# Kernel optimization log

Hardware: AMD Instinct MI355X
Metric: run time of the kernel (lower is better)

Reference implementation:

```python
import jax, jax.numpy as jnp
import numpy as np

B, S, H = 2, 1024, 2048
E, F = 16, 1024          # num_experts, moe_intermediate_size
TOP_K = 4
SH_F = 5632              # shared_expert_intermediate_size


def setup_inputs() -> dict:
    key = jax.random.key(0)
    ks = jax.random.split(key, 9)
    sc = 0.02
    return {
        'hidden_states': jax.random.normal(ks[0], (B, S, H), dtype=jnp.float32),
        'w_router': jax.random.normal(ks[1], (H, E), dtype=jnp.float32) * sc,
        'w_gate': jax.random.normal(ks[2], (E, H, F), dtype=jnp.float32) * sc,
        'w_up': jax.random.normal(ks[3], (E, H, F), dtype=jnp.float32) * sc,
        'w_down': jax.random.normal(ks[4], (E, F, H), dtype=jnp.float32) * sc,
        'w_sh_gate': jax.random.normal(ks[5], (H, SH_F), dtype=jnp.float32) * sc,
        'w_sh_up': jax.random.normal(ks[6], (H, SH_F), dtype=jnp.float32) * sc,
        'w_sh_down': jax.random.normal(ks[7], (SH_F, H), dtype=jnp.float32) * sc,
        'w_sh_expert_gate': jax.random.normal(ks[8], (H, 1), dtype=jnp.float32) * sc,
    }


def reference(hidden_states, w_router, w_gate, w_up, w_down,
              w_sh_gate, w_sh_up, w_sh_down, w_sh_expert_gate):
    b, s, h = hidden_states.shape
    x = hidden_states.reshape(-1, h)                      # [T, H]

    # router: softmax over all experts, then top-k, renormalize (norm_topk_prob=True)
    router_logits = x @ w_router                          # [T, E]
    probs = jax.nn.softmax(router_logits, axis=-1)
    topk_w, topk_ids = jax.lax.top_k(probs, TOP_K)        # [T, k]
    topk_w = topk_w / jnp.sum(topk_w, axis=-1, keepdims=True)

    # combine matrix [T, E]: routing weight per (token, expert)
    combine = jnp.sum(
        jax.nn.one_hot(topk_ids, E, dtype=x.dtype) * topk_w[..., None], axis=1)

    # experts: SwiGLU per expert, weighted-combined before down projection
    g = jnp.einsum('th,ehf->tef', x, w_gate)              # [T, E, F]
    u = jnp.einsum('th,ehf->tef', x, w_up)
    act = jax.nn.silu(g) * u                              # SiluAndMul
    act = act * combine[:, :, None]                       # fold routing weights
    moe_out = jnp.einsum('tef,efh->th', act, w_down)      # [T, H]

    # shared expert with sigmoid gate
    sg = jax.nn.silu(x @ w_sh_gate) * (x @ w_sh_up)       # [T, SH_F]
    shared = sg @ w_sh_down                               # [T, H]
    gate = jax.nn.sigmoid(x @ w_sh_expert_gate)           # [T, 1]
    out = moe_out + gate * shared
    return out.reshape(b, s, h)
```

## Files before the change

kernel.cpp:

```cpp
#include <hip/hip_runtime.h>
#include <hip/hip_bf16.h>
#include <stdint.h>

#define T_TOK 2048
#define HD    2048
#define NE    16
#define FF    1024
#define TOPK  4
#define SHF   5632

typedef __attribute__((ext_vector_type(8))) short short8;
typedef __attribute__((ext_vector_type(4))) float f32x4;

typedef const __attribute__((address_space(1))) uint32_t* gp1_t;
typedef __attribute__((address_space(3))) uint32_t* lp3_t;

__device__ __forceinline__ void gload_lds16(const void* g, void* l) {
  __builtin_amdgcn_global_load_lds((gp1_t)g, (lp3_t)l, 16, 0, 0);
}

__device__ __forceinline__ unsigned short f2bf(float f) {
  __hip_bfloat16 h = __float2bfloat16(f);
  return __builtin_bit_cast(unsigned short, h);
}
__device__ __forceinline__ float bf2f(unsigned short u) {
  return __uint_as_float(((uint32_t)u) << 16);
}

__global__ __launch_bounds__(256) void k_prep(const float* __restrict__ x,
                                              unsigned short* __restrict__ xb,
                                              float* __restrict__ out,
                                              int* __restrict__ counts, int n) {
  int i = blockIdx.x * blockDim.x + threadIdx.x;
  int stride = gridDim.x * blockDim.x;
  for (; i < n; i += stride) { xb[i] = f2bf(x[i]); out[i] = 0.f; }
  if (blockIdx.x == 0 && threadIdx.x < NE) counts[threadIdx.x] = 0;
}

__global__ __launch_bounds__(256) void k_transpose(const float* __restrict__ src,
    unsigned short* __restrict__ dst, int K, int N) {
  __shared__ unsigned short tile[64][72];
  const int k0 = blockIdx.x * 64;
  const int n0 = blockIdx.y * 64;
  const size_t boff = (size_t)blockIdx.z * K * N;
  src += boff; dst += boff;
  const int t = threadIdx.x;
  const int c4 = (t & 15) * 4;
  const int kr0 = (t >> 4) * 4;
#pragma unroll
  for (int j = 0; j < 4; ++j) {
    int kr = kr0 + j;
    float4 v = *(const float4*)(src + (size_t)(k0 + kr) * N + n0 + c4);
    tile[c4 + 0][kr] = f2bf(v.x);
    tile[c4 + 1][kr] = f2bf(v.y);
    tile[c4 + 2][kr] = f2bf(v.z);
    tile[c4 + 3][kr] = f2bf(v.w);
  }
  __syncthreads();
  const int nr = t >> 2;
  const int kc = (t & 3) * 8;
  unsigned short* orow = dst + (size_t)(n0 + nr) * K + k0;
  *(short8*)(orow + kc)      = *(const short8*)(&tile[nr][kc]);
  *(short8*)(orow + kc + 32) = *(const short8*)(&tile[nr][kc + 32]);
}

__global__ __launch_bounds__(64) void k_router(
    const float* __restrict__ x, const float* __restrict__ wr,
    const float* __restrict__ wsg, int* __restrict__ counts,
    int* __restrict__ list, float* __restrict__ wlist,
    float* __restrict__ gate_sh) {
  const int t = blockIdx.x;
  const int lane = threadIdx.x;
  const float* xrow = x + (size_t)t * HD;
  float p[NE + 1];
#pragma unroll
  for (int e = 0; e <= NE; ++e) p[e] = 0.f;
  for (int i = lane; i < HD; i += 64) {
    float xv = xrow[i];
    const float* wrow = wr + (size_t)i * NE;
#pragma unroll
    for (int e = 0; e < NE; ++e) p[e] += xv * wrow[e];
    p[NE] += xv * wsg[i];
  }
#pragma unroll
  for (int e = 0; e <= NE; ++e) {
    float v = p[e];
    for (int off = 32; off; off >>= 1) v += __shfl_xor(v, off);
    p[e] = v;
  }
  if (lane == 0) {
    gate_sh[t] = 1.f / (1.f + __expf(-p[NE]));
    float l[NE];
#pragma unroll
    for (int e = 0; e < NE; ++e) l[e] = p[e];
    int ids[TOPK]; float lg[TOPK];
#pragma unroll
    for (int k = 0; k < TOPK; ++k) {
      int best = 0; float bv = l[0];
#pragma unroll
      for (int e = 1; e < NE; ++e) { if (l[e] > bv) { bv = l[e]; best = e; } }
      ids[k] = best; lg[k] = bv; l[best] = -1e30f;
    }
    float m = lg[0], s = 0.f, w[TOPK];
#pragma unroll
    for (int k = 0; k < TOPK; ++k) { w[k] = __expf(lg[k] - m); s += w[k]; }
    float inv = 1.f / s;
#pragma unroll
    for (int k = 0; k < TOPK; ++k) {
      int e = ids[k];
      int pos = atomicAdd(&counts[e], 1);
      list[e * T_TOK + pos] = t;
      wlist[e * T_TOK + pos] = w[k] * inv;
    }
  }
}

__global__ __launch_bounds__(256) void k_offsets(
    const int* __restrict__ counts, int* __restrict__ offsets,
    const float* __restrict__ wlist, float* __restrict__ wpair) {
  __shared__ int soff[NE];
  if (threadIdx.x == 0) {
    int off = 0;
    for (int e = 0; e < NE; ++e) { offsets[e] = off; soff[e] = off; off += counts[e]; }
    offsets[NE] = off;
  }
  __syncthreads();
  for (int idx = threadIdx.x; idx < NE * T_TOK; idx += 256) {
    int e = idx >> 11, pos = idx & (T_TOK - 1);
    if (pos < counts[e]) wpair[soff[e] + pos] = wlist[idx];
  }
}

template<int MODE>
__global__ __launch_bounds__(256, 2) void k_gemm(
    const unsigned short* __restrict__ A, int lda, int nkt,
    const unsigned short* __restrict__ B0, const unsigned short* __restrict__ B1,
    int nsplit, size_t strideB, int ldb,
    unsigned short* __restrict__ O0, unsigned short* __restrict__ O1, int ldo,
    float* __restrict__ OF,
    const int* __restrict__ offsets, const int* __restrict__ counts,
    const int* __restrict__ list, const float* __restrict__ gate_sh)
{
  __shared__ unsigned short lds[2][2 * 8192];
  __shared__ int tokLDS[128];

  const int cb = blockIdx.x, rb = blockIdx.y;
  const int e = (MODE <= 1) ? blockIdx.z : 0;
  const int tid = threadIdx.x, l = tid & 63, wid = tid >> 6;
  const int wr = wid >> 1, wc = wid & 1;

  int cnt = T_TOK;
  if (MODE <= 1) {
    cnt = counts[e];
    if (rb * 128 >= cnt) return;
  }
  if (MODE == 0) {
    if (tid < 128) {
      int r = rb * 128 + tid;
      tokLDS[tid] = list[e * T_TOK + (r < cnt ? r : cnt - 1)];
    }
    __syncthreads();
  }

  const int swz8 = ((l & 7) ^ (l >> 3)) * 8;
  const unsigned short* Bsel = (cb < nsplit) ? B0 : B1;
  const int cb2 = (cb < nsplit) ? cb : cb - nsplit;
  const size_t eoff = (MODE <= 1) ? (size_t)e * strideB : (size_t)0;

  const unsigned short* aS[4];
  const unsigned short* bS[4];
#pragma unroll
  for (int i = 0; i < 4; ++i) {
    int rloc = wid * 32 + i * 8 + (l >> 3);
    int arow;
    if (MODE == 0) arow = tokLDS[rloc];
    else if (MODE == 1) { int rr = rb * 128 + rloc; if (rr >= cnt) rr = cnt - 1; arow = offsets[e] + rr; }
    else arow = rb * 128 + rloc;
    aS[i] = A + (size_t)arow * lda + swz8;
    bS[i] = Bsel + eoff + (size_t)(cb2 * 128 + rloc) * ldb + swz8;
  }

  auto STAGE = [&](int kt) {
    unsigned short* base = &lds[kt & 1][0] + (wid * 32) * 64;
    const int k0 = kt * 64;
#pragma unroll
    for (int i = 0; i < 4; ++i) {
      gload_lds16(aS[i] + k0, base + i * 8 * 64);
      gload_lds16(bS[i] + k0, base + i * 8 * 64 + 8192);
    }
  };

  f32x4 acc[4][4];
#pragma unroll
  for (int mf = 0; mf < 4; ++mf)
#pragma unroll
    for (int nf = 0; nf < 4; ++nf) acc[mf][nf] = (f32x4){0.f, 0.f, 0.f, 0.f};

  STAGE(0);

  for (int kt = 0; kt < nkt; ++kt) {
    if (kt + 1 < nkt) {
      STAGE(kt + 1);
      asm volatile("s_waitcnt vmcnt(8)" ::: "memory");
    } else {
      asm volatile("s_waitcnt vmcnt(0)" ::: "memory");
    }
    __builtin_amdgcn_s_barrier();
    asm volatile("" ::: "memory");

    const char* lAb = (const char*)&lds[kt & 1][0];
    const char* lBb = lAb + 16384;
#pragma unroll
    for (int kk = 0; kk < 2; ++kk) {
      const int kb = kk * 64 + ((l >> 4) * 16);
      short8 af[4], bf[4];
#pragma unroll
      for (int mf = 0; mf < 4; ++mf) {
        int row = wr * 64 + mf * 16 + (l & 15);
        af[mf] = *(const short8*)(lAb + row * 128 + (kb ^ ((row & 7) << 4)));
      }
#pragma unroll
      for (int nf = 0; nf < 4; ++nf) {
        int n = wc * 64 + nf * 16 + (l & 15);
        bf[nf] = *(const short8*)(lBb + n * 128 + (kb ^ ((n & 7) << 4)));
      }
      __builtin_amdgcn_s_setprio(1);
#pragma unroll
      for (int mf = 0; mf < 4; ++mf)
#pragma unroll
        for (int nf = 0; nf < 4; ++nf)
          acc[mf][nf] = __builtin_amdgcn_mfma_f32_16x16x32_bf16(af[mf], bf[nf], acc[mf][nf], 0, 0, 0);
      __builtin_amdgcn_s_setprio(0);
    }
    asm volatile("" ::: "memory");
    __builtin_amdgcn_s_barrier();
    asm volatile("" ::: "memory");
  }

  const int g4 = (l >> 4) * 4;
  const int cL = l & 15;
  const int colb = cb2 * 128 + wc * 64 + cL;

  if constexpr (MODE == 0) {
    unsigned short* Out = (cb < nsplit) ? O0 : O1;
    const int obase = offsets[e];
#pragma unroll
    for (int mf = 0; mf < 4; ++mf)
#pragma unroll
      for (int r = 0; r < 4; ++r) {
        int rloc = rb * 128 + wr * 64 + mf * 16 + g4 + r;
        if (rloc < cnt) {
          size_t orow = (size_t)(obase + rloc) * ldo + colb;
#pragma unroll
          for (int nf = 0; nf < 4; ++nf)
            Out[orow + nf * 16] = f2bf(acc[mf][nf][r]);
        }
      }
  } else if constexpr (MODE == 2) {
    unsigned short* Out = (cb < nsplit) ? O0 : O1;
#pragma unroll
    for (int mf = 0; mf < 4; ++mf)
#pragma unroll
      for (int r = 0; r < 4; ++r) {
        int rloc = rb * 128 + wr * 64 + mf * 16 + g4 + r;
        size_t orow = (size_t)rloc * ldo + colb;
#pragma unroll
        for (int nf = 0; nf < 4; ++nf)
          Out[orow + nf * 16] = f2bf(acc[mf][nf][r]);
      }
  } else if constexpr (MODE == 1) {
#pragma unroll
    for (int mf = 0; mf < 4; ++mf)
#pragma unroll
      for (int r = 0; r < 4; ++r) {
        int rloc = rb * 128 + wr * 64 + mf * 16 + g4 + r;
        if (rloc < cnt) {
          int tok = list[e * T_TOK + rloc];
          float* dst = OF + (size_t)tok * HD + colb;
#pragma unroll
          for (int nf = 0; nf < 4; ++nf)
            atomicAdd(dst + nf * 16, acc[mf][nf][r]);
        }
      }
  } else {
#pragma unroll
    for (int mf = 0; mf < 4; ++mf)
#pragma unroll
      for (int r = 0; r < 4; ++r) {
        int rloc = rb * 128 + wr * 64 + mf * 16 + g4 + r;
        float g = gate_sh[rloc];
        float* dst = OF + (size_t)rloc * HD + colb;
#pragma unroll
        for (int nf = 0; nf < 4; ++nf)
          dst[nf * 16] += g * acc[mf][nf][r];
      }
  }
}

__global__ __launch_bounds__(256) void k_silu(
    unsigned short* __restrict__ gq, const unsigned short* __restrict__ uq,
    const float* __restrict__ wrow, long total)
{
  long i = ((long)blockIdx.x * blockDim.x + threadIdx.x) * 4;
  const long stride = (long)gridDim.x * blockDim.x * 4;
  for (; i < total; i += stride) {
    ushort4 gv = *(const ushort4*)(gq + i);
    ushort4 uv = *(const ushort4*)(uq + i);
    float w = wrow ? wrow[i >> 10] : 1.f;
    float a0 = bf2f(gv.x), a1 = bf2f(gv.y), a2 = bf2f(gv.z), a3 = bf2f(gv.w);
    float b0 = bf2f(uv.x), b1 = bf2f(uv.y), b2 = bf2f(uv.z), b3 = bf2f(uv.w);
    ushort4 o;
    o.x = f2bf(a0 / (1.f + __expf(-a0)) * b0 * w);
    o.y = f2bf(a1 / (1.f + __expf(-a1)) * b1 * w);
    o.z = f2bf(a2 / (1.f + __expf(-a2)) * b2 * w);
    o.w = f2bf(a3 / (1.f + __expf(-a3)) * b3 * w);
    *(ushort4*)(gq + i) = o;
  }
}

extern "C" void kernel_launch(void* const* d_in, const int* in_sizes, int n_in,
                              void* d_out, int out_size, void* d_ws, size_t ws_size,
                              hipStream_t stream) {
  const float* x     = (const float*)d_in[0];
  const float* wrout = (const float*)d_in[1];
  const float* wgate = (const float*)d_in[2];
  const float* wup   = (const float*)d_in[3];
  const float* wdown = (const float*)d_in[4];
  const float* wsg   = (const float*)d_in[5];
  const float* wsu   = (const float*)d_in[6];
  const float* wsd   = (const float*)d_in[7];
  const float* wseg  = (const float*)d_in[8];
  float* out = (float*)d_out;

  char* ws = (char*)d_ws;
  unsigned short* xb = (unsigned short*)ws;
  char* region1 = ws + (size_t)(8u << 20);
  unsigned short* actg = (unsigned short*)region1;
  unsigned short* actu = (unsigned short*)(region1 + (size_t)(16u << 20));
  unsigned short* sgg  = (unsigned short*)region1;
  unsigned short* sgu  = (unsigned short*)(region1 + (size_t)23068672);
  char* p3 = region1 + (size_t)46137344;
  int*   counts  = (int*)p3;
  int*   offsets = (int*)(p3 + 256);
  float* gateS   = (float*)(p3 + 512);
  float* wpair   = (float*)(p3 + 512 + 8192);
  int*   list    = (int*)(p3 + 512 + 8192 + 32768);
  float* wlist   = (float*)(p3 + 512 + 8192 + 32768 + 131072);
  char* p4 = p3 + (size_t)(1u << 20);
  unsigned short* W1 = (unsigned short*)p4;
  unsigned short* W2 = (unsigned short*)(p4 + (size_t)(64u << 20));
  (void)ws_size; (void)in_sizes; (void)n_in; (void)out_size;

  const int n = T_TOK * HD;
  k_prep<<<dim3(4096), dim3(256), 0, stream>>>(x, xb, out, counts, n);
  k_router<<<dim3(T_TOK), dim3(64), 0, stream>>>(x, wrout, wseg, counts, list, wlist, gateS);
  k_offsets<<<dim3(1), dim3(256), 0, stream>>>(counts, offsets, wlist, wpair);

  k_transpose<<<dim3(32, 16, 16), dim3(256), 0, stream>>>(wgate, W1, HD, FF);
  k_transpose<<<dim3(32, 16, 16), dim3(256), 0, stream>>>(wup,   W2, HD, FF);

  k_gemm<0><<<dim3(16, 16, 16), dim3(256), 0, stream>>>(
      xb, HD, 32, W1, W2, 8, (size_t)HD * FF, HD,
      actg, actu, FF, (float*)nullptr, offsets, counts, list, (const float*)nullptr);
  k_silu<<<dim3(4096), dim3(256), 0, stream>>>(actg, actu, wpair, (long)T_TOK * TOPK * FF);

  k_transpose<<<dim3(16, 32, 16), dim3(256), 0, stream>>>(wdown, W1, FF, HD);
  k_gemm<1><<<dim3(16, 16, 16), dim3(256), 0, stream>>>(
      actg, FF, 16, W1, W1, 1 << 30, (size_t)FF * HD, FF,
      (unsigned short*)nullptr, (unsigned short*)nullptr, HD,
      out, offsets, counts, list, (const float*)nullptr);

  unsigned short* WsgT = W2;
  unsigned short* WsuT = W2 + (size_t)SHF * HD;
  k_transpose<<<dim3(32, 88, 1), dim3(256), 0, stream>>>(wsg, WsgT, HD, SHF);
  k_transpose<<<dim3(32, 88, 1), dim3(256), 0, stream>>>(wsu, WsuT, HD, SHF);

  k_gemm<2><<<dim3(88, 16, 1), dim3(256), 0, stream>>>(
      xb, HD, 32, WsgT, WsuT, 44, (size_t)0, HD,
      sgg, sgu, SHF, (float*)nullptr, offsets, counts, list, (const float*)nullptr);
  k_silu<<<dim3(4096), dim3(256), 0, stream>>>(sgg, sgu, (const float*)nullptr, (long)T_TOK * SHF);

  k_transpose<<<dim3(88, 32, 1), dim3(256), 0, stream>>>(wsd, W1, SHF, HD);
  k_gemm<3><<<dim3(16, 16, 1), dim3(256), 0, stream>>>(
      sgg, SHF, 88, W1, W1, 1 << 30, (size_t)0, SHF,
      (unsigned short*)nullptr, (unsigned short*)nullptr, HD,
      out, offsets, counts, list, gateS);
}
```

Before: 709.8 us.

## Fuse SiLU into up-projection GEMM epilogue and reorder shared/routed expert stages

The two standalone SiLU-multiply kernels are removed. Gate and up projections now run as separate GEMM launches, and the up GEMM's epilogue reads the stored gate result, applies silu(g)*u, and scales by the routing weight. The shared expert now runs first and writes `out` directly instead of accumulating, so the zero-fill in prep goes away and the routed experts then atomically add on top. The gate/up GEMMs drop double buffering and the occupancy hint, using a single LDS buffer with __syncthreads. This trades the elementwise passes and the out-zeroing for an extra GEMM launch, a re-read of the gate tensor, and possibly less load/compute overlap in those GEMMs.

```diff
diff --git a/kernel.cpp b/kernel.cpp
--- a/kernel.cpp
+++ b/kernel.cpp
@@ -29,11 +29,10 @@
 
 __global__ __launch_bounds__(256) void k_prep(const float* __restrict__ x,
                                               unsigned short* __restrict__ xb,
-                                              float* __restrict__ out,
                                               int* __restrict__ counts, int n) {
   int i = blockIdx.x * blockDim.x + threadIdx.x;
   int stride = gridDim.x * blockDim.x;
-  for (; i < n; i += stride) { xb[i] = f2bf(x[i]); out[i] = 0.f; }
+  for (; i < n; i += stride) xb[i] = f2bf(x[i]);
   if (blockIdx.x == 0 && threadIdx.x < NE) counts[threadIdx.x] = 0;
 }
 
@@ -131,17 +130,19 @@
   }
 }
 
-template<int MODE>
-__global__ __launch_bounds__(256, 2) void k_gemm(
-    const unsigned short* __restrict__ A, int lda, int nkt,
-    const unsigned short* __restrict__ B0, const unsigned short* __restrict__ B1,
-    int nsplit, size_t strideB, int ldb,
-    unsigned short* __restrict__ O0, unsigned short* __restrict__ O1, int ldo,
+template<int MODE, int ACT>
+__global__ __launch_bounds__(256) void k_gemm(
+    const unsigned short* __restrict__ A, int lda, int K,
+    const unsigned short* __restrict__ B, size_t strideB,
+    const unsigned short* __restrict__ GPREV,
+    unsigned short* __restrict__ O, int ldo,
     float* __restrict__ OF,
-    const int* __restrict__ offsets, const int* __restrict__ counts,
-    const int* __restrict__ list, const float* __restrict__ gate_sh)
+    const int* __restrict__ counts, const int* __restrict__ offsets,
+    const int* __restrict__ list, const float* __restrict__ wrow,
+    const float* __restrict__ gate_sh)
 {
-  __shared__ unsigned short lds[2][2 * 8192];
+  constexpr bool DBUF = (MODE == 1 || MODE == 3);
+  __shared__ unsigned short lds[DBUF ? 2 * 16384 : 16384];
   __shared__ int tokLDS[128];
 
   const int cb = blockIdx.x, rb = blockIdx.y;
@@ -163,8 +164,6 @@
   }
 
   const int swz8 = ((l & 7) ^ (l >> 3)) * 8;
-  const unsigned short* Bsel = (cb < nsplit) ? B0 : B1;
-  const int cb2 = (cb < nsplit) ? cb : cb - nsplit;
   const size_t eoff = (MODE <= 1) ? (size_t)e * strideB : (size_t)0;
 
   const unsigned short* aS[4];
@@ -177,96 +176,127 @@
     else if (MODE == 1) { int rr = rb * 128 + rloc; if (rr >= cnt) rr = cnt - 1; arow = offsets[e] + rr; }
     else arow = rb * 128 + rloc;
     aS[i] = A + (size_t)arow * lda + swz8;
-    bS[i] = Bsel + eoff + (size_t)(cb2 * 128 + rloc) * ldb + swz8;
-  }
-
-  auto STAGE = [&](int kt) {
-    unsigned short* base = &lds[kt & 1][0] + (wid * 32) * 64;
-    const int k0 = kt * 64;
-#pragma unroll
-    for (int i = 0; i < 4; ++i) {
-      gload_lds16(aS[i] + k0, base + i * 8 * 64);
-      gload_lds16(bS[i] + k0, base + i * 8 * 64 + 8192);
+    bS[i] = B + eoff + (size_t)(cb * 128 + rloc) * K + swz8;
+  }
+
+  f32x4 acc[4][4];
+#pragma unroll
+  for (int mf = 0; mf < 4; ++mf)
+#pragma unroll
+    for (int nf = 0; nf < 4; ++nf) acc[mf][nf] = (f32x4){0.f, 0.f, 0.f, 0.f};
+
+  const int nkt = K / 64;
+
+  if constexpr (!DBUF) {
+    for (int kt = 0; kt < nkt; ++kt) {
+      const int k0 = kt * 64;
+      unsigned short* base = &lds[0] + (wid * 32) * 64;
+#pragma unroll
+      for (int i = 0; i < 4; ++i) {
+        gload_lds16(aS[i] + k0, base + i * 8 * 64);
+        gload_lds16(bS[i] + k0, base + i * 8 * 64 + 8192);
+      }
+      __syncthreads();
+      const char* lAb = (const char*)&lds[0];
+      const char* lBb = lAb + 16384;
+#pragma unroll
+      for (int kk = 0; kk < 2; ++kk) {
+        const int kb = kk * 64 + ((l >> 4) * 16);
+        short8 af[4], bf[4];
+#pragma unroll
+        for (int mf = 0; mf < 4; ++mf) {
+          int row = wr * 64 + mf * 16 + (l & 15);
+          af[mf] = *(const short8*)(lAb + row * 128 + (kb ^ ((row & 7) << 4)));
+        }
+#pragma unroll
+        for (int nf = 0; nf < 4; ++nf) {
+          int n = wc * 64 + nf * 16 + (l & 15);
+          bf[nf] = *(const short8*)(lBb + n * 128 + (kb ^ ((n & 7) << 4)));
+        }
+#pragma unroll
+        for (int mf = 0; mf < 4; ++mf)
+#pragma unroll
+          for (int nf = 0; nf < 4; ++nf)
+            acc[mf][nf] = __builtin_amdgcn_mfma_f32_16x16x32_bf16(af[mf], bf[nf], acc[mf][nf], 0, 0, 0);
+      }
+      __syncthreads();
     }
-  };
-
-  f32x4 acc[4][4];
-#pragma unroll
-  for (int mf = 0; mf < 4; ++mf)
-#pragma unroll
-    for (int nf = 0; nf < 4; ++nf) acc[mf][nf] = (f32x4){0.f, 0.f, 0.f, 0.f};
-
-  STAGE(0);
-
-  for (int kt = 0; kt < nkt; ++kt) {
-    if (kt + 1 < nkt) {
-      STAGE(kt + 1);
-      asm volatile("s_waitcnt vmcnt(8)" ::: "memory");
-    } else {
-      asm volatile("s_waitcnt vmcnt(0)" ::: "memory");
+  } else {
+    auto STAGE = [&](int kt) {
+      unsigned short* base = &lds[0] + (kt & 1) * 16384 + (wid * 32) * 64;
+      const int k0 = kt * 64;
+#pragma unroll
+      for (int i = 0; i < 4; ++i) {
+        gload_lds16(aS[i] + k0, base + i * 8 * 64);
+        gload_lds16(bS[i] + k0, base + i * 8 * 64 + 8192);
+      }
+    };
+    STAGE(0);
+    for (int kt = 0; kt < nkt; ++kt) {
+      if (kt + 1 < nkt) {
+        STAGE(kt + 1);
+        asm volatile("s_waitcnt vmcnt(8)" ::: "memory");
+      } else {
+        asm volatile("s_waitcnt vmcnt(0)" ::: "memory");
+      }
+      __builtin_amdgcn_s_barrier();
+      asm volatile("" ::: "memory");
+      const char* lAb = (const char*)(&lds[0] + (kt & 1) * 16384);
+      const char* lBb = lAb + 16384;
+#pragma unroll
+      for (int kk = 0; kk < 2; ++kk) {
+        const int kb = kk * 64 + ((l >> 4) * 16);
+        short8 af[4], bf[4];
+#pragma unroll
+        for (int mf = 0; mf < 4; ++mf) {
+          int row = wr * 64 + mf * 16 + (l & 15);
+          af[mf] = *(const short8*)(lAb + row * 128 + (kb ^ ((row & 7) << 4)));
+        }
+#pragma unroll
+        for (int nf = 0; nf < 4; ++nf) {
+          int n = wc * 64 + nf * 16 + (l & 15);
+          bf[nf] = *(const short8*)(lBb + n * 128 + (kb ^ ((n & 7) << 4)));
+        }
+        __builtin_amdgcn_s_setprio(1);
+#pragma unroll
+        for (int mf = 0; mf < 4; ++mf)
+#pragma unroll
+          for (int nf = 0; nf < 4; ++nf)
+            acc[mf][nf] = __builtin_amdgcn_mfma_f32_16x16x32_bf16(af[mf], bf[nf], acc[mf][nf], 0, 0, 0);
+        __builtin_amdgcn_s_setprio(0);
+      }
+      asm volatile("" ::: "memory");
+      __builtin_amdgcn_s_barrier();
+      asm volatile("" ::: "memory");
     }
-    __builtin_amdgcn_s_barrier();
-    asm volatile("" ::: "memory");
-
-    const char* lAb = (const char*)&lds[kt & 1][0];
-    const char* lBb = lAb + 16384;
-#pragma unroll
-    for (int kk = 0; kk < 2; ++kk) {
-      const int kb = kk * 64 + ((l >> 4) * 16);
-      short8 af[4], bf[4];
-#pragma unroll
-      for (int mf = 0; mf < 4; ++mf) {
-        int row = wr * 64 + mf * 16 + (l & 15);
-        af[mf] = *(const short8*)(lAb + row * 128 + (kb ^ ((row & 7) << 4)));
-      }
-#pragma unroll
-      for (int nf = 0; nf < 4; ++nf) {
-        int n = wc * 64 + nf * 16 + (l & 15);
-        bf[nf] = *(const short8*)(lBb + n * 128 + (kb ^ ((n & 7) << 4)));
-      }
-      __builtin_amdgcn_s_setprio(1);
-#pragma unroll
-      for (int mf = 0; mf < 4; ++mf)
-#pragma unroll
-        for (int nf = 0; nf < 4; ++nf)
-          acc[mf][nf] = __builtin_amdgcn_mfma_f32_16x16x32_bf16(af[mf], bf[nf], acc[mf][nf], 0, 0, 0);
-      __builtin_amdgcn_s_setprio(0);
-    }
-    asm volatile("" ::: "memory");
-    __builtin_amdgcn_s_barrier();
-    asm volatile("" ::: "memory");
   }
 
   const int g4 = (l >> 4) * 4;
   const int cL = l & 15;
-  const int colb = cb2 * 128 + wc * 64 + cL;
-
-  if constexpr (MODE == 0) {
-    unsigned short* Out = (cb < nsplit) ? O0 : O1;
-    const int obase = offsets[e];
+  const int colb = cb * 128 + wc * 64;
+
+  if constexpr (MODE == 0 || MODE == 2) {
+    const int obase = (MODE == 0) ? offsets[e] : 0;
 #pragma unroll
     for (int mf = 0; mf < 4; ++mf)
 #pragma unroll
       for (int r = 0; r < 4; ++r) {
         int rloc = rb * 128 + wr * 64 + mf * 16 + g4 + r;
-        if (rloc < cnt) {
-          size_t orow = (size_t)(obase + rloc) * ldo + colb;
+        if (MODE == 0 && rloc >= cnt) continue;
+        size_t orow = (size_t)(obase + rloc) * ldo + colb;
+        if constexpr (ACT == 0) {
 #pragma unroll
           for (int nf = 0; nf < 4; ++nf)
-            Out[orow + nf * 16] = f2bf(acc[mf][nf][r]);
-        }
-      }
-  } else if constexpr (MODE == 2) {
-    unsigned short* Out = (cb < nsplit) ? O0 : O1;
-#pragma unroll
-    for (int mf = 0; mf < 4; ++mf)
-#pragma unroll
-      for (int r = 0; r < 4; ++r) {
-        int rloc = rb * 128 + wr * 64 + mf * 16 + g4 + r;
-        size_t orow = (size_t)rloc * ldo + colb;
-#pragma unroll
-        for (int nf = 0; nf < 4; ++nf)
-          Out[orow + nf * 16] = f2bf(acc[mf][nf][r]);
+            O[orow + nf * 16 + cL] = f2bf(acc[mf][nf][r]);
+        } else {
+          float w = (MODE == 0) ? wrow[obase + rloc] : 1.f;
+#pragma unroll
+          for (int nf = 0; nf < 4; ++nf) {
+            float g = bf2f(GPREV[orow + nf * 16 + cL]);
+            float u = acc[mf][nf][r];
+            O[orow + nf * 16 + cL] = f2bf(g / (1.f + __expf(-g)) * u * w);
+          }
+        }
       }
   } else if constexpr (MODE == 1) {
 #pragma unroll
@@ -279,7 +309,7 @@
           float* dst = OF + (size_t)tok * HD + colb;
 #pragma unroll
           for (int nf = 0; nf < 4; ++nf)
-            atomicAdd(dst + nf * 16, acc[mf][nf][r]);
+            atomicAdd(dst + nf * 16 + cL, acc[mf][nf][r]);
         }
       }
   } else {
@@ -287,34 +317,13 @@
     for (int mf = 0; mf < 4; ++mf)
 #pragma unroll
       for (int r = 0; r < 4; ++r) {
-        int rloc = rb * 128 + wr * 64 + mf * 16 + g4 + r;
-        float g = gate_sh[rloc];
-        float* dst = OF + (size_t)rloc * HD + colb;
+        int t = rb * 128 + wr * 64 + mf * 16 + g4 + r;
+        float g = gate_sh[t];
+        float* dst = OF + (size_t)t * HD + colb;
 #pragma unroll
         for (int nf = 0; nf < 4; ++nf)
-          dst[nf * 16] += g * acc[mf][nf][r];
-      }
-  }
-}
-
-__global__ __launch_bounds__(256) void k_silu(
-    unsigned short* __restrict__ gq, const unsigned short* __restrict__ uq,
-    const float* __restrict__ wrow, long total)
-{
-  long i = ((long)blockIdx.x * blockDim.x + threadIdx.x) * 4;
-  const long stride = (long)gridDim.x * blockDim.x * 4;
-  for (; i < total; i += stride) {
-    ushort4 gv = *(const ushort4*)(gq + i);
-    ushort4 uv = *(const ushort4*)(uq + i);
-    float w = wrow ? wrow[i >> 10] : 1.f;
-    float a0 = bf2f(gv.x), a1 = bf2f(gv.y), a2 = bf2f(gv.z), a3 = bf2f(gv.w);
-    float b0 = bf2f(uv.x), b1 = bf2f(uv.y), b2 = bf2f(uv.z), b3 = bf2f(uv.w);
-    ushort4 o;
-    o.x = f2bf(a0 / (1.f + __expf(-a0)) * b0 * w);
-    o.y = f2bf(a1 / (1.f + __expf(-a1)) * b1 * w);
-    o.z = f2bf(a2 / (1.f + __expf(-a2)) * b2 * w);
-    o.w = f2bf(a3 / (1.f + __expf(-a3)) * b3 * w);
-    *(ushort4*)(gq + i) = o;
+          dst[nf * 16 + cL] = g * acc[mf][nf][r];
+      }
   }
 }
 
@@ -335,10 +344,10 @@
   char* ws = (char*)d_ws;
   unsigned short* xb = (unsigned short*)ws;
   char* region1 = ws + (size_t)(8u << 20);
+  unsigned short* sgg  = (unsigned short*)region1;
+  unsigned short* sgu  = (unsigned short*)(region1 + (size_t)23068672);
   unsigned short* actg = (unsigned short*)region1;
   unsigned short* actu = (unsigned short*)(region1 + (size_t)(16u << 20));
-  unsigned short* sgg  = (unsigned short*)region1;
-  unsigned short* sgu  = (unsigned short*)(region1 + (size_t)23068672);
   char* p3 = region1 + (size_t)46137344;
   int*   counts  = (int*)p3;
   int*   offsets = (int*)(p3 + 256);
@@ -352,37 +361,45 @@
   (void)ws_size; (void)in_sizes; (void)n_in; (void)out_size;
 
   const int n = T_TOK * HD;
-  k_prep<<<dim3(4096), dim3(256), 0, stream>>>(x, xb, out, counts, n);
+  k_prep<<<dim3(2048), dim3(256), 0, stream>>>(x, xb, counts, n);
   k_router<<<dim3(T_TOK), dim3(64), 0, stream>>>(x, wrout, wseg, counts, list, wlist, gateS);
   k_offsets<<<dim3(1), dim3(256), 0, stream>>>(counts, offsets, wlist, wpair);
-
-  k_transpose<<<dim3(32, 16, 16), dim3(256), 0, stream>>>(wgate, W1, HD, FF);
-  k_transpose<<<dim3(32, 16, 16), dim3(256), 0, stream>>>(wup,   W2, HD, FF);
-
-  k_gemm<0><<<dim3(16, 16, 16), dim3(256), 0, stream>>>(
-      xb, HD, 32, W1, W2, 8, (size_t)HD * FF, HD,
-      actg, actu, FF, (float*)nullptr, offsets, counts, list, (const float*)nullptr);
-  k_silu<<<dim3(4096), dim3(256), 0, stream>>>(actg, actu, wpair, (long)T_TOK * TOPK * FF);
-
-  k_transpose<<<dim3(16, 32, 16), dim3(256), 0, stream>>>(wdown, W1, FF, HD);
-  k_gemm<1><<<dim3(16, 16, 16), dim3(256), 0, stream>>>(
-      actg, FF, 16, W1, W1, 1 << 30, (size_t)FF * HD, FF,
-      (unsigned short*)nullptr, (unsigned short*)nullptr, HD,
-      out, offsets, counts, list, (const float*)nullptr);
 
   unsigned short* WsgT = W2;
   unsigned short* WsuT = W2 + (size_t)SHF * HD;
   k_transpose<<<dim3(32, 88, 1), dim3(256), 0, stream>>>(wsg, WsgT, HD, SHF);
   k_transpose<<<dim3(32, 88, 1), dim3(256), 0, stream>>>(wsu, WsuT, HD, SHF);
 
-  k_gemm<2><<<dim3(88, 16, 1), dim3(256), 0, stream>>>(
-      xb, HD, 32, WsgT, WsuT, 44, (size_t)0, HD,
-      sgg, sgu, SHF, (float*)nullptr, offsets, counts, list, (const float*)nullptr);
-  k_silu<<<dim3(4096), dim3(256), 0, stream>>>(sgg, sgu, (const float*)nullptr, (long)T_TOK * SHF);
+  k_gemm<2, 0><<<dim3(44, 16), dim3(256), 0, stream>>>(
+      xb, HD, HD, WsgT, (size_t)0, (const unsigned short*)nullptr,
+      sgg, SHF, (float*)nullptr, counts, offsets, list,
+      (const float*)nullptr, (const float*)nullptr);
+  k_gemm<2, 1><<<dim3(44, 16), dim3(256), 0, stream>>>(
+      xb, HD, HD, WsuT, (size_t)0, sgg,
+      sgu, SHF, (float*)nullptr, counts, offsets, list,
+      (const float*)nullptr, (const float*)nullptr);
 
   k_transpose<<<dim3(88, 32, 1), dim3(256), 0, stream>>>(wsd, W1, SHF, HD);
-  k_gemm<3><<<dim3(16, 16, 1), dim3(256), 0, stream>>>(
-      sgg, SHF, 88, W1, W1, 1 << 30, (size_t)0, SHF,
-      (unsigned short*)nullptr, (unsigned short*)nullptr, HD,
-      out, offsets, counts, list, gateS);
-}
+  k_gemm<3, 0><<<dim3(16, 16), dim3(256), 0, stream>>>(
+      sgu, SHF, SHF, W1, (size_t)0, (const unsigned short*)nullptr,
+      (unsigned short*)nullptr, HD, out, counts, offsets, list,
+      (const float*)nullptr, gateS);
+
+  k_transpose<<<dim3(32, 16, 16), dim3(256), 0, stream>>>(wgate, W1, HD, FF);
+  k_transpose<<<dim3(32, 16, 16), dim3(256), 0, stream>>>(wup,   W2, HD, FF);
+
+  k_gemm<0, 0><<<dim3(8, 16, 16), dim3(256), 0, stream>>>(
+      xb, HD, HD, W1, (size_t)HD * FF, (const unsigned short*)nullptr,
+      actg, FF, (float*)nullptr, counts, offsets, list,
+      (const float*)nullptr, (const float*)nullptr);
+  k_gemm<0, 1><<<dim3(8, 16, 16), dim3(256), 0, stream>>>(
+      xb, HD, HD, W2, (size_t)HD * FF, actg,
+      actu, FF, (float*)nullptr, counts, offsets, list,
+      wpair, (const float*)nullptr);
+
+  k_transpose<<<dim3(16, 32, 16), dim3(256), 0, stream>>>(wdown, W1, FF, HD);
+  k_gemm<1, 0><<<dim3(16, 16, 16), dim3(256), 0, stream>>>(
+      actu, FF, FF, W1, (size_t)FF * HD, (const unsigned short*)nullptr,
+      (unsigned short*)nullptr, HD, out, counts, offsets, list,
+      (const float*)nullptr, (const float*)nullptr);
+}
```

Result: slower. 739.2 us (+4.1%).
